# Kernel optimization log

Measured on AMD Instinct MI355X. Metric: run time of the kernel, lower is better.

## Reference

```python
import jax, jax.numpy as jnp
import numpy as np

N = 8388608      # number of points
S = 32768        # number of superpoints (segments)


def setup_inputs() -> dict:
    key = jax.random.key(0)
    k1, k2, k3 = jax.random.split(key, 3)
    pos = jax.random.normal(k1, (N, 3), dtype=jnp.float32)
    idx = jnp.sort(jax.random.randint(k2, (N,), 0, S, dtype=jnp.int64))
    w = jax.random.uniform(k3, (N,), dtype=jnp.float32)  # non-negative weights
    return {"pos": pos, "idx": idx, "w": w, "num_super": S}


def reference(pos, idx, w, num_super):
    # Per-segment min / max of coordinates: [S, 3]
    mn = jax.ops.segment_min(pos, idx, num_segments=num_super, indices_are_sorted=True)
    mx = jax.ops.segment_max(pos, idx, num_segments=num_super, indices_are_sorted=True)
    # Per-segment diameter = largest coordinate extent: [S]
    diameter_segment = (mx - mn).max(axis=1)
    # Weighted per-segment center: sum(w*pos) / sum(w), guarding zero-weight segments
    w_sum = jax.ops.segment_sum(w, idx, num_segments=num_super, indices_are_sorted=True)
    w_sum_safe = jnp.where(w_sum == 0, 1.0, w_sum)
    center_segment = (
        jax.ops.segment_sum(pos * w[:, None], idx, num_segments=num_super,
                            indices_are_sorted=True)
        / w_sum_safe[:, None]
    )
    # Gather per-node center/diameter and normalize into unit sphere
    pos_out = (pos - center_segment[idx]) / (diameter_segment[idx][:, None] + 0.01)
    return pos_out, diameter_segment.reshape(-1, 1)
```

## Files before the change

kernel.cpp:

```cpp
#include <hip/hip_runtime.h>

#define WAVE 64
#define WPB 2

__global__ void detect_idx64(const unsigned int* __restrict__ w32, long long N,
                             int* __restrict__ flag) {
    long long base = (N / 2) | 1LL;
    long long stride = ((N / 2) / 64) & ~1LL;
    if (stride < 2) stride = 2;
    long long p = base + (long long)threadIdx.x * stride;
    unsigned int v = (p < N) ? w32[p] : 0u;
    unsigned long long nz = __ballot(v != 0u);
    if (threadIdx.x == 0) *flag = (nz == 0ULL) ? 1 : 0;
}

__device__ __forceinline__ int load_idx(const void* __restrict__ p,
                                        long long i, int is64) {
    return is64 ? (int)((const long long*)p)[i] : ((const int*)p)[i];
}

__global__ void find_bounds_bs(const void* __restrict__ idxp,
                               const int* __restrict__ flag,
                               int* __restrict__ start,
                               long long N, int S) {
    const int t = blockIdx.x * blockDim.x + threadIdx.x;
    if (t > S) return;
    const int is64 = *flag;
    long long lo = 0, hi = N;
    while (lo < hi) {
        long long mid = (lo + hi) >> 1;
        if (load_idx(idxp, mid, is64) < t) lo = mid + 1; else hi = mid;
    }
    start[t] = (int)lo;
}

__global__ __launch_bounds__(WPB * WAVE)
void seg_norm(const float* __restrict__ pos,
              const float* __restrict__ w,
              const int* __restrict__ start,
              float* __restrict__ out,
              float* __restrict__ diam_out,
              int S) {
    const int s = blockIdx.x * WPB + (threadIdx.x >> 6);
    if (s >= S) return;
    const int lane = threadIdx.x & 63;

    const int lo = start[s], hi = start[s + 1];
    const int g0 = lo >> 2, g1 = (hi + 3) >> 2;

    const float4* __restrict__ pos4 = (const float4*)pos;
    const float4* __restrict__ w4   = (const float4*)w;

    const int ga = g0 + lane;
    const int gb = ga + WAVE;
    const bool va = ga < g1, vb = gb < g1;

    float4 a0 = {0,0,0,0}, a1 = {0,0,0,0}, a2 = {0,0,0,0}, aw = {0,0,0,0};
    float4 b0 = {0,0,0,0}, b1 = {0,0,0,0}, b2 = {0,0,0,0}, bw = {0,0,0,0};
    if (va) {
        a0 = pos4[3LL * ga]; a1 = pos4[3LL * ga + 1]; a2 = pos4[3LL * ga + 2];
        aw = w4[ga];
    }
    if (vb) {
        b0 = pos4[3LL * gb]; b1 = pos4[3LL * gb + 1]; b2 = pos4[3LL * gb + 2];
        bw = w4[gb];
    }

    float mnx = INFINITY,  mny = INFINITY,  mnz = INFINITY;
    float mxx = -INFINITY, mxy = -INFINITY, mxz = -INFINITY;
    float sw = 0.f, swx = 0.f, swy = 0.f, swz = 0.f;

    #define PROC(PI, X, Y, Z, WV)                                        \
    {                                                                    \
        bool in = ((PI) >= lo) & ((PI) < hi);                            \
        float xv = (X), yv = (Y), zv = (Z);                              \
        float wv = in ? (WV) : 0.f;                                      \
        mnx = fminf(mnx, in ? xv :  INFINITY);                           \
        mxx = fmaxf(mxx, in ? xv : -INFINITY);                           \
        mny = fminf(mny, in ? yv :  INFINITY);                           \
        mxy = fmaxf(mxy, in ? yv : -INFINITY);                           \
        mnz = fminf(mnz, in ? zv :  INFINITY);                           \
        mxz = fmaxf(mxz, in ? zv : -INFINITY);                           \
        sw += wv;                                                        \
        swx = fmaf(wv, xv, swx);                                         \
        swy = fmaf(wv, yv, swy);                                         \
        swz = fmaf(wv, zv, swz);                                         \
    }
    #define PROC_GROUP(G, R0, R1, R2, RW)                                \
    {                                                                    \
        const int p = (G) << 2;                                          \
        PROC(p + 0, R0.x, R0.y, R0.z, RW.x)                              \
        PROC(p + 1, R0.w, R1.x, R1.y, RW.y)                              \
        PROC(p + 2, R1.z, R1.w, R2.x, RW.z)                              \
        PROC(p + 3, R2.y, R2.z, R2.w, RW.w)                              \
    }

    PROC_GROUP(ga, a0, a1, a2, aw)
    PROC_GROUP(gb, b0, b1, b2, bw)

    for (int g = g0 + 2 * WAVE + lane; g < g1; g += WAVE) {
        float4 c0 = pos4[3LL * g], c1 = pos4[3LL * g + 1], c2 = pos4[3LL * g + 2];
        float4 cw = w4[g];
        PROC_GROUP(g, c0, c1, c2, cw)
    }

    #pragma unroll
    for (int off = 1; off < WAVE; off <<= 1) {
        mnx = fminf(mnx, __shfl_xor(mnx, off));
        mny = fminf(mny, __shfl_xor(mny, off));
        mnz = fminf(mnz, __shfl_xor(mnz, off));
        mxx = fmaxf(mxx, __shfl_xor(mxx, off));
        mxy = fmaxf(mxy, __shfl_xor(mxy, off));
        mxz = fmaxf(mxz, __shfl_xor(mxz, off));
        sw  += __shfl_xor(sw,  off);
        swx += __shfl_xor(swx, off);
        swy += __shfl_xor(swy, off);
        swz += __shfl_xor(swz, off);
    }

    const float diam = fmaxf(mxx - mnx, fmaxf(mxy - mny, mxz - mnz));
    const float wsafe = (sw == 0.f) ? 1.f : sw;
    const float cx = swx / wsafe, cy = swy / wsafe, cz = swz / wsafe;
    const float inv = 1.f / (diam + 0.01f);
    if (lane == 0) diam_out[s] = diam;

    float4* __restrict__ out4 = (float4*)out;

    #define STORE_GROUP(G, R0, R1, R2)                                       \
    {                                                                        \
        const int p = (G) << 2;                                              \
        float4 ra, rb, rc;                                                   \
        ra.x = (R0.x - cx) * inv; ra.y = (R0.y - cy) * inv;                  \
        ra.z = (R0.z - cz) * inv; ra.w = (R0.w - cx) * inv;                  \
        rb.x = (R1.x - cy) * inv; rb.y = (R1.y - cz) * inv;                  \
        rb.z = (R1.z - cx) * inv; rb.w = (R1.w - cy) * inv;                  \
        rc.x = (R2.x - cz) * inv; rc.y = (R2.y - cx) * inv;                  \
        rc.z = (R2.z - cy) * inv; rc.w = (R2.w - cz) * inv;                  \
        if (p >= lo && p + 4 <= hi) {                                        \
            out4[3LL * (G)] = ra; out4[3LL * (G) + 1] = rb;                  \
            out4[3LL * (G) + 2] = rc;                                        \
        } else {                                                             \
            const long long f = 12LL * (G);                                  \
            if (p + 0 >= lo && p + 0 < hi) {                                 \
                out[f + 0] = ra.x; out[f + 1]  = ra.y; out[f + 2]  = ra.z;   \
            }                                                                \
            if (p + 1 >= lo && p + 1 < hi) {                                 \
                out[f + 3] = ra.w; out[f + 4]  = rb.x; out[f + 5]  = rb.y;   \
            }                                                                \
            if (p + 2 >= lo && p + 2 < hi) {                                 \
                out[f + 6] = rb.z; out[f + 7]  = rb.w; out[f + 8]  = rc.x;   \
            }                                                                \
            if (p + 3 >= lo && p + 3 < hi) {                                 \
                out[f + 9] = rc.y; out[f + 10] = rc.z; out[f + 11] = rc.w;   \
            }                                                                \
        }                                                                    \
    }

    STORE_GROUP(ga, a0, a1, a2)
    STORE_GROUP(gb, b0, b1, b2)

    for (int g = g0 + 2 * WAVE + lane; g < g1; g += WAVE) {
        float4 c0 = pos4[3LL * g], c1 = pos4[3LL * g + 1], c2 = pos4[3LL * g + 2];
        STORE_GROUP(g, c0, c1, c2)
    }

    #undef STORE_GROUP
    #undef PROC_GROUP
    #undef PROC
}

extern "C" void kernel_launch(void* const* d_in, const int* in_sizes, int n_in,
                              void* d_out, int out_size, void* d_ws, size_t ws_size,
                              hipStream_t stream) {
    const float* pos  = (const float*)d_in[0];
    const void*  idxp = d_in[1];
    const float* w    = (const float*)d_in[2];

    const long long N = (long long)in_sizes[0] / 3;
    const int S = out_size - in_sizes[0];

    float* out = (float*)d_out;
    float* diam_out = out + (long long)in_sizes[0];

    int* flag  = (int*)d_ws;
    int* start = (int*)((char*)d_ws + 256);

    detect_idx64<<<1, 64, 0, stream>>>((const unsigned int*)idxp, N, flag);

    find_bounds_bs<<<(S + 1 + 63) / 64, 64, 0, stream>>>(idxp, flag, start, N, S);

    seg_norm<<<(S + WPB - 1) / WPB, WPB * WAVE, 0, stream>>>(
        pos, w, start, out, diam_out, S);
}
```

Baseline: 57.13 us.

## Process four segments per wave with software-prefetched next-segment loads

Each wavefront now handles four consecutive segments instead of one. It loads all five boundaries with a single lane-parallel read plus shuffles, and prefetches the next segment's first chunk into a double-buffered register set while the current segment is reduced and stored. The aim is to hide global load latency across the serialized reduce-then-store phases and to cut per-wave launch and boundary-load overhead. The cost is higher register pressure and four times fewer blocks, which can reduce occupancy and parallelism when segments are only a few hundred points long.

```diff
diff --git a/kernel.cpp b/kernel.cpp
--- a/kernel.cpp
+++ b/kernel.cpp
@@ -2,6 +2,7 @@
 
 #define WAVE 64
 #define WPB 2
+#define SPW 4
 
 __global__ void detect_idx64(const unsigned int* __restrict__ w32, long long N,
                              int* __restrict__ flag) {
@@ -41,38 +42,37 @@
               float* __restrict__ out,
               float* __restrict__ diam_out,
               int S) {
-    const int s = blockIdx.x * WPB + (threadIdx.x >> 6);
-    if (s >= S) return;
+    const int wid  = threadIdx.x >> 6;
     const int lane = threadIdx.x & 63;
-
-    const int lo = start[s], hi = start[s + 1];
-    const int g0 = lo >> 2, g1 = (hi + 3) >> 2;
+    const int s0 = (blockIdx.x * WPB + wid) * SPW;
+    if (s0 >= S) return;
+
+    int k = s0 + (lane < SPW ? lane : SPW);
+    if (k > S) k = S;
+    const int bv = start[k];
+    const int e0 = __shfl(bv, 0), e1 = __shfl(bv, 1), e2 = __shfl(bv, 2),
+              e3 = __shfl(bv, 3), e4 = __shfl(bv, 4);
 
     const float4* __restrict__ pos4 = (const float4*)pos;
     const float4* __restrict__ w4   = (const float4*)w;
-
-    const int ga = g0 + lane;
-    const int gb = ga + WAVE;
-    const bool va = ga < g1, vb = gb < g1;
-
-    float4 a0 = {0,0,0,0}, a1 = {0,0,0,0}, a2 = {0,0,0,0}, aw = {0,0,0,0};
-    float4 b0 = {0,0,0,0}, b1 = {0,0,0,0}, b2 = {0,0,0,0}, bw = {0,0,0,0};
-    if (va) {
-        a0 = pos4[3LL * ga]; a1 = pos4[3LL * ga + 1]; a2 = pos4[3LL * ga + 2];
-        aw = w4[ga];
-    }
-    if (vb) {
-        b0 = pos4[3LL * gb]; b1 = pos4[3LL * gb + 1]; b2 = pos4[3LL * gb + 2];
-        bw = w4[gb];
-    }
-
-    float mnx = INFINITY,  mny = INFINITY,  mnz = INFINITY;
-    float mxx = -INFINITY, mxy = -INFINITY, mxz = -INFINITY;
-    float sw = 0.f, swx = 0.f, swy = 0.f, swz = 0.f;
-
-    #define PROC(PI, X, Y, Z, WV)                                        \
+    float4* __restrict__ out4 = (float4*)out;
+
+    float4 PA_0 = {0,0,0,0}, PA_1 = {0,0,0,0}, PA_2 = {0,0,0,0}, PA_w = {0,0,0,0};
+    float4 PB_0 = {0,0,0,0}, PB_1 = {0,0,0,0}, PB_2 = {0,0,0,0}, PB_w = {0,0,0,0};
+    float4 BB_0 = {0,0,0,0}, BB_1 = {0,0,0,0}, BB_2 = {0,0,0,0}, BB_w = {0,0,0,0};
+
+    {
+        const int ng0 = e0 >> 2, ng1 = (e1 + 3) >> 2;
+        const int nga = ng0 + lane;
+        if (nga < ng1) {
+            PA_0 = pos4[3LL * nga]; PA_1 = pos4[3LL * nga + 1];
+            PA_2 = pos4[3LL * nga + 2]; PA_w = w4[nga];
+        }
+    }
+
+    #define PROC(PI, LO, HI, X, Y, Z, WV)                                \
     {                                                                    \
-        bool in = ((PI) >= lo) & ((PI) < hi);                            \
+        bool in = ((PI) >= (LO)) & ((PI) < (HI));                        \
         float xv = (X), yv = (Y), zv = (Z);                              \
         float wv = in ? (WV) : 0.f;                                      \
         mnx = fminf(mnx, in ? xv :  INFINITY);                           \
@@ -86,49 +86,17 @@
         swy = fmaf(wv, yv, swy);                                         \
         swz = fmaf(wv, zv, swz);                                         \
     }
-    #define PROC_GROUP(G, R0, R1, R2, RW)                                \
+    #define PROC_GROUP(G, LO, HI, R0, R1, R2, RW)                        \
     {                                                                    \
-        const int p = (G) << 2;                                          \
-        PROC(p + 0, R0.x, R0.y, R0.z, RW.x)                              \
-        PROC(p + 1, R0.w, R1.x, R1.y, RW.y)                              \
-        PROC(p + 2, R1.z, R1.w, R2.x, RW.z)                              \
-        PROC(p + 3, R2.y, R2.z, R2.w, RW.w)                              \
-    }
-
-    PROC_GROUP(ga, a0, a1, a2, aw)
-    PROC_GROUP(gb, b0, b1, b2, bw)
-
-    for (int g = g0 + 2 * WAVE + lane; g < g1; g += WAVE) {
-        float4 c0 = pos4[3LL * g], c1 = pos4[3LL * g + 1], c2 = pos4[3LL * g + 2];
-        float4 cw = w4[g];
-        PROC_GROUP(g, c0, c1, c2, cw)
-    }
-
-    #pragma unroll
-    for (int off = 1; off < WAVE; off <<= 1) {
-        mnx = fminf(mnx, __shfl_xor(mnx, off));
-        mny = fminf(mny, __shfl_xor(mny, off));
-        mnz = fminf(mnz, __shfl_xor(mnz, off));
-        mxx = fmaxf(mxx, __shfl_xor(mxx, off));
-        mxy = fmaxf(mxy, __shfl_xor(mxy, off));
-        mxz = fmaxf(mxz, __shfl_xor(mxz, off));
-        sw  += __shfl_xor(sw,  off);
-        swx += __shfl_xor(swx, off);
-        swy += __shfl_xor(swy, off);
-        swz += __shfl_xor(swz, off);
-    }
-
-    const float diam = fmaxf(mxx - mnx, fmaxf(mxy - mny, mxz - mnz));
-    const float wsafe = (sw == 0.f) ? 1.f : sw;
-    const float cx = swx / wsafe, cy = swy / wsafe, cz = swz / wsafe;
-    const float inv = 1.f / (diam + 0.01f);
-    if (lane == 0) diam_out[s] = diam;
-
-    float4* __restrict__ out4 = (float4*)out;
-
-    #define STORE_GROUP(G, R0, R1, R2)                                       \
+        const int p_ = (G) << 2;                                         \
+        PROC(p_ + 0, LO, HI, R0.x, R0.y, R0.z, RW.x)                     \
+        PROC(p_ + 1, LO, HI, R0.w, R1.x, R1.y, RW.y)                     \
+        PROC(p_ + 2, LO, HI, R1.z, R1.w, R2.x, RW.z)                     \
+        PROC(p_ + 3, LO, HI, R2.y, R2.z, R2.w, RW.w)                     \
+    }
+    #define STORE_GROUP(G, LO, HI, R0, R1, R2)                               \
     {                                                                        \
-        const int p = (G) << 2;                                              \
+        const int p_ = (G) << 2;                                             \
         float4 ra, rb, rc;                                                   \
         ra.x = (R0.x - cx) * inv; ra.y = (R0.y - cy) * inv;                  \
         ra.z = (R0.z - cz) * inv; ra.w = (R0.w - cx) * inv;                  \
@@ -136,34 +104,88 @@
         rb.z = (R1.z - cx) * inv; rb.w = (R1.w - cy) * inv;                  \
         rc.x = (R2.x - cz) * inv; rc.y = (R2.y - cx) * inv;                  \
         rc.z = (R2.z - cy) * inv; rc.w = (R2.w - cz) * inv;                  \
-        if (p >= lo && p + 4 <= hi) {                                        \
+        if (p_ >= (LO) && p_ + 4 <= (HI)) {                                  \
             out4[3LL * (G)] = ra; out4[3LL * (G) + 1] = rb;                  \
             out4[3LL * (G) + 2] = rc;                                        \
         } else {                                                             \
             const long long f = 12LL * (G);                                  \
-            if (p + 0 >= lo && p + 0 < hi) {                                 \
+            if (p_ + 0 >= (LO) && p_ + 0 < (HI)) {                           \
                 out[f + 0] = ra.x; out[f + 1]  = ra.y; out[f + 2]  = ra.z;   \
             }                                                                \
-            if (p + 1 >= lo && p + 1 < hi) {                                 \
+            if (p_ + 1 >= (LO) && p_ + 1 < (HI)) {                           \
                 out[f + 3] = ra.w; out[f + 4]  = rb.x; out[f + 5]  = rb.y;   \
             }                                                                \
-            if (p + 2 >= lo && p + 2 < hi) {                                 \
+            if (p_ + 2 >= (LO) && p_ + 2 < (HI)) {                           \
                 out[f + 6] = rb.z; out[f + 7]  = rb.w; out[f + 8]  = rc.x;   \
             }                                                                \
-            if (p + 3 >= lo && p + 3 < hi) {                                 \
+            if (p_ + 3 >= (LO) && p_ + 3 < (HI)) {                           \
                 out[f + 9] = rc.y; out[f + 10] = rc.z; out[f + 11] = rc.w;   \
             }                                                                \
         }                                                                    \
     }
 
-    STORE_GROUP(ga, a0, a1, a2)
-    STORE_GROUP(gb, b0, b1, b2)
-
-    for (int g = g0 + 2 * WAVE + lane; g < g1; g += WAVE) {
-        float4 c0 = pos4[3LL * g], c1 = pos4[3LL * g + 1], c2 = pos4[3LL * g + 2];
-        STORE_GROUP(g, c0, c1, c2)
-    }
-
+    #define SEG_ITER(SIDX, CUR, NXT, LO, HI, NLO, NHI, PF)                   \
+    {                                                                        \
+        const int g0 = (LO) >> 2, g1 = ((HI) + 3) >> 2;                      \
+        const int ga = g0 + lane, gb = ga + WAVE;                            \
+        const bool vb = gb < g1;                                             \
+        const bool anyb = __any(vb);                                         \
+        if (vb) {                                                            \
+            BB_0 = pos4[3LL * gb]; BB_1 = pos4[3LL * gb + 1];                \
+            BB_2 = pos4[3LL * gb + 2]; BB_w = w4[gb];                        \
+        }                                                                    \
+        if (PF) {                                                            \
+            const int ng0 = (NLO) >> 2, ng1 = ((NHI) + 3) >> 2;              \
+            const int nga = ng0 + lane;                                      \
+            if (nga < ng1) {                                                 \
+                NXT##0 = pos4[3LL * nga]; NXT##1 = pos4[3LL * nga + 1];      \
+                NXT##2 = pos4[3LL * nga + 2]; NXT##w = w4[nga];              \
+            }                                                                \
+        }                                                                    \
+        float mnx = INFINITY,  mny = INFINITY,  mnz = INFINITY;              \
+        float mxx = -INFINITY, mxy = -INFINITY, mxz = -INFINITY;             \
+        float sw = 0.f, swx = 0.f, swy = 0.f, swz = 0.f;                     \
+        PROC_GROUP(ga, LO, HI, CUR##0, CUR##1, CUR##2, CUR##w)               \
+        if (anyb) PROC_GROUP(gb, LO, HI, BB_0, BB_1, BB_2, BB_w)             \
+        for (int g = g0 + 2 * WAVE + lane; g < g1; g += WAVE) {              \
+            float4 c0 = pos4[3LL * g], c1 = pos4[3LL * g + 1],               \
+                   c2 = pos4[3LL * g + 2];                                   \
+            float4 cw = w4[g];                                               \
+            PROC_GROUP(g, LO, HI, c0, c1, c2, cw)                            \
+        }                                                                    \
+        _Pragma("unroll")                                                    \
+        for (int off = 1; off < WAVE; off <<= 1) {                           \
+            mnx = fminf(mnx, __shfl_xor(mnx, off));                          \
+            mny = fminf(mny, __shfl_xor(mny, off));                          \
+            mnz = fminf(mnz, __shfl_xor(mnz, off));                          \
+            mxx = fmaxf(mxx, __shfl_xor(mxx, off));                          \
+            mxy = fmaxf(mxy, __shfl_xor(mxy, off));                          \
+            mxz = fmaxf(mxz, __shfl_xor(mxz, off));                          \
+            sw  += __shfl_xor(sw,  off);                                     \
+            swx += __shfl_xor(swx, off);                                     \
+            swy += __shfl_xor(swy, off);                                     \
+            swz += __shfl_xor(swz, off);                                     \
+        }                                                                    \
+        const float diam = fmaxf(mxx - mnx, fmaxf(mxy - mny, mxz - mnz));    \
+        const float wsafe = (sw == 0.f) ? 1.f : sw;                          \
+        const float cx = swx / wsafe, cy = swy / wsafe, cz = swz / wsafe;    \
+        const float inv = 1.f / (diam + 0.01f);                              \
+        if (lane == 0 && (SIDX) < S) diam_out[SIDX] = diam;                  \
+        STORE_GROUP(ga, LO, HI, CUR##0, CUR##1, CUR##2)                      \
+        if (anyb) STORE_GROUP(gb, LO, HI, BB_0, BB_1, BB_2)                  \
+        for (int g = g0 + 2 * WAVE + lane; g < g1; g += WAVE) {              \
+            float4 c0 = pos4[3LL * g], c1 = pos4[3LL * g + 1],               \
+                   c2 = pos4[3LL * g + 2];                                   \
+            STORE_GROUP(g, LO, HI, c0, c1, c2)                               \
+        }                                                                    \
+    }
+
+    SEG_ITER(s0 + 0, PA_, PB_, e0, e1, e1, e2, 1)
+    SEG_ITER(s0 + 1, PB_, PA_, e1, e2, e2, e3, 1)
+    SEG_ITER(s0 + 2, PA_, PB_, e2, e3, e3, e4, 1)
+    SEG_ITER(s0 + 3, PB_, PA_, e3, e4, 0, 0, 0)
+
+    #undef SEG_ITER
     #undef STORE_GROUP
     #undef PROC_GROUP
     #undef PROC
@@ -189,6 +211,7 @@
 
     find_bounds_bs<<<(S + 1 + 63) / 64, 64, 0, stream>>>(idxp, flag, start, N, S);
 
-    seg_norm<<<(S + WPB - 1) / WPB, WPB * WAVE, 0, stream>>>(
+    const int segs_per_block = WPB * SPW;
+    seg_norm<<<(S + segs_per_block - 1) / segs_per_block, WPB * WAVE, 0, stream>>>(
         pos, w, start, out, diam_out, S);
 }
```

New measurement: 60.35 us. 5.6% more time.
